# Performance work log

Measured on AMD Instinct MI355X. Metric: run time of the kernel, lower is better.

## Reference

```python
import jax, jax.numpy as jnp
import numpy as np

EPS = 1e-12  # F.normalize default eps (denominator = max(norm, eps))


def setup_inputs() -> dict:
    key = jax.random.key(0)
    ks = jax.random.split(key, 8)
    B, FIN, H, W = 4, 256, 64, 64
    N_MEM, SQ = 64, 16           # sqrt_fin = fin**0.5
    POS_CH = 2                    # PosEncoding concatenates one coord channel per dim
    CIN = FIN + POS_CH
    QK = N_MEM * SQ               # 1024
    # PosEncoding buffer: normalized coordinate grid in [-1, 1], shape [2, H, W]
    ys = jnp.linspace(-1.0, 1.0, H, dtype=jnp.float32)
    xs = jnp.linspace(-1.0, 1.0, W, dtype=jnp.float32)
    gy, gx = jnp.meshgrid(ys, xs, indexing='ij')
    pos = jnp.stack([gy, gx], axis=0)
    s = 0.02
    return {
        'x':    jax.random.normal(ks[0], (B, FIN, H, W), jnp.float32),
        'pos':  pos,
        'wq':   jax.random.normal(ks[1], (QK, CIN), jnp.float32) * s,
        'bq':   jnp.zeros((QK,), jnp.float32),
        'wk':   jax.random.normal(ks[2], (QK, CIN), jnp.float32) * s,
        'bk':   jnp.zeros((QK,), jnp.float32),
        'v':    jax.random.normal(ks[3], (N_MEM, FIN), jnp.float32) * s,
        'wout': jax.random.normal(ks[4], (FIN, FIN), jnp.float32) * s,
        'bout': jnp.zeros((FIN,), jnp.float32),
    }


def reference(x, pos, wq, bq, wk, bk, v, wout, bout):
    B, C, H, W = x.shape
    S = H * W
    n_mem, fin = v.shape
    sq = wq.shape[0] // n_mem
    # PosEncoding: concat coordinate channels
    posb = jnp.broadcast_to(pos[None], (B,) + pos.shape)
    xp = jnp.concatenate([x, posb], axis=1).reshape(B, C + pos.shape[0], S)
    # 1x1 conv projections (channel GEMMs)
    q = jnp.einsum('oc,bcs->bos', wq, xp) + bq[None, :, None]  # [B, n_mem*sq, S]
    k = jnp.einsum('oc,bcs->bos', wk, xp) + bk[None, :, None]
    q = q.reshape(B, n_mem, sq, S).transpose(0, 3, 1, 2)  # [B,S,m,sq]
    k = k.reshape(B, n_mem, sq, S).transpose(0, 3, 2, 1)  # [B,S,sq,m]
    # F.normalize: q over last dim (sqrt_fin), k over dim=1 (sqrt_fin)
    qn = q / jnp.maximum(jnp.linalg.norm(q, axis=-1, keepdims=True), EPS)
    kn = k / jnp.maximum(jnp.linalg.norm(k, axis=2, keepdims=True), EPS)
    # attn[b,s,m,n] = qn . kn ; dropout is identity in eval mode.
    # mean over memory slots m commutes with (attn @ v), so fuse:
    attn_mean = jnp.einsum('bsk,bskn->bsn', qn.mean(axis=2), kn)  # [B,S,n_mem]
    mem = attn_mean @ v                                            # [B,S,fin]
    mem = mem.transpose(0, 2, 1).reshape(B, fin, H, W)
    out = jnp.einsum('of,bfhw->bohw', wout, mem) + bout[None, :, None, None]
    return x + out
```

## Files before the change

kernel.cpp:

```cpp
#include <hip/hip_runtime.h>
#include <stdint.h>

#define EPSN 1e-12f

typedef float f32x16 __attribute__((ext_vector_type(16)));
typedef float f32x4 __attribute__((ext_vector_type(4)));
typedef __bf16 bf16x8 __attribute__((ext_vector_type(8)));

__device__ __forceinline__ unsigned short f2bf(float f) {
  union { float f; unsigned int u; } v; v.f = f;
  unsigned int u = v.u + 0x7FFFu + ((v.u >> 16) & 1u);
  return (unsigned short)(u >> 16);
}

#define NKS 17
#define WQF_OFF 0
#define WKF_OFF (32 * NKS * 64 * 8)
#define WVP_OFF (2 * 32 * NKS * 64 * 8)

__global__ __launch_bounds__(256) void prep_kernel(
    const float* __restrict__ wq, const float* __restrict__ bq,
    const float* __restrict__ wk, const float* __restrict__ bk,
    const float* __restrict__ v, const float* __restrict__ wout,
    unsigned short* __restrict__ wsp) {
  int bid = blockIdx.x;
  if (bid < 512) {
    int isK = bid >= 256;
    int ob = (bid & 255) * 4;
    const float* w = isK ? wk : wq;
    const float* bb = isK ? bk : bq;
    unsigned short* dst = wsp + (isK ? WKF_OFF : WQF_OFF);
    for (int i = threadIdx.x; i < 4 * 129; i += 256) {
      int r = i / 129, q = i - r * 129;
      int o = ob + r, k = q * 2;
      float2 w2 = *(const float2*)(w + o * 258 + k);
      int g = o >> 5, col = o & 31;
      int ks = k >> 4, hi = (k >> 3) & 1, j = k & 7;
      uint32_t pk = (uint32_t)f2bf(w2.x) | ((uint32_t)f2bf(w2.y) << 16);
      *(uint32_t*)(dst + (((g * NKS + ks) * 64 + hi * 32 + col) << 3) + j) = pk;
    }
    for (int i = threadIdx.x; i < 4 * 14; i += 256) {
      int r = i / 14, kk = 258 + (i - r * 14);
      int o = ob + r;
      int g = o >> 5, col = o & 31;
      int ks = kk >> 4, hi = (kk >> 3) & 1, j = kk & 7;
      dst[(((g * NKS + ks) * 64 + hi * 32 + col) << 3) + j] =
          (kk == 258) ? f2bf(bb[o]) : (unsigned short)0;
    }
  } else {
    int idx = (bid - 512) * 256 + threadIdx.x;
    int fc = idx & 15, m = (idx >> 4) & 63, o = idx >> 10;
    const f32x4* wo = (const f32x4*)(wout + o * 256 + fc * 16);
    const f32x4* vm = (const f32x4*)(v + m * 256 + fc * 16);
    float s = 0.f;
#pragma unroll
    for (int f = 0; f < 4; ++f) {
      f32x4 a = wo[f], bvv = vm[f];
      s += a[0]*bvv[0] + a[1]*bvv[1] + a[2]*bvv[2] + a[3]*bvv[3];
    }
    s += __shfl_xor(s, 1, 64);
    s += __shfl_xor(s, 2, 64);
    s += __shfl_xor(s, 4, 64);
    s += __shfl_xor(s, 8, 64);
    if (fc == 0) wsp[WVP_OFF + o * 64 + m] = f2bf(s);
  }
}

#define PXB 32
#define KP 296
#define QS 34
#define AT 76

__global__ __launch_bounds__(1024, 8) void fused_kernel(
    const float* __restrict__ x, const float* __restrict__ pos,
    const unsigned short* __restrict__ wsp, const float* __restrict__ bout,
    float* __restrict__ out) {
  __shared__ __align__(16) unsigned short xp[PXB * KP];
  __shared__ __align__(16) float qbarL[16 * QS];
  __shared__ __align__(16) unsigned short attnM[PXB * AT];
  __shared__ float boutL[256];

  const int tid = threadIdx.x;
  const int lane = tid & 63;
  const int wid = __builtin_amdgcn_readfirstlane(tid >> 6);
  const int px = lane & 31, q2 = lane >> 5;
  const int P0 = blockIdx.x * PXB;
  const int b = P0 >> 12, s0 = P0 & 4095;

  const int wtoff = (2 * wid) * NKS * 512 + lane * 8;
  const unsigned short* wqf = wsp + WQF_OFF + wtoff;
  const unsigned short* wkf = wsp + WKF_OFF + wtoff;

  uint32_t* xp32 = (uint32_t*)xp;
  {
    const float* xrow = x + b * 256 * 4096 + s0;
    float v0[4], v1[4];
#pragma unroll
    for (int it = 0; it < 4; ++it) {
      int item = tid + it * 1024;
      int pp = item & 31, dcol = item >> 5;
      v0[it] = xrow[(2 * dcol) * 4096 + pp];
      v1[it] = xrow[(2 * dcol + 1) * 4096 + pp];
    }
#pragma unroll
    for (int it = 0; it < 4; ++it) {
      int item = tid + it * 1024;
      int pp = item & 31, dcol = item >> 5;
      xp32[pp * 148 + dcol] =
          (uint32_t)f2bf(v0[it]) | ((uint32_t)f2bf(v1[it]) << 16);
    }
    if (tid < 256) {
      int pp = tid & 31, dcol = 128 + (tid >> 5);
      float t0 = 0.f, t1 = 0.f;
      if (dcol == 128) { t0 = pos[s0 + pp]; t1 = pos[4096 + s0 + pp]; }
      else if (dcol == 129) { t0 = 1.0f; }
      xp32[pp * 148 + dcol] = (uint32_t)f2bf(t0) | ((uint32_t)f2bf(t1) << 16);
    }
  }
  if (tid < 256) boutL[tid] = bout[tid];
  for (int i = tid; i < 16 * QS; i += 1024) qbarL[i] = 0.f;
  __syncthreads();

#define PHASE(WB) do {                                                    \
    _Pragma("unroll")                                                     \
    for (int ks = 0; ks < NKS; ++ks) {                                    \
      bf16x8 _A0 = *(const bf16x8*)((WB) + ks * 512);                     \
      bf16x8 _A1 = *(const bf16x8*)((WB) + NKS * 512 + ks * 512);         \
      bf16x8 _b0 = *(const bf16x8*)&xp[px * KP + ks * 16 + q2 * 8];       \
      acc0 = __builtin_amdgcn_mfma_f32_32x32x16_bf16(_A0, _b0, acc0, 0, 0, 0); \
      acc1 = __builtin_amdgcn_mfma_f32_32x32x16_bf16(_A1, _b0, acc1, 0, 0, 0); \
    }                                                                     \
  } while (0)

  f32x16 acc0 = (f32x16)0.f, acc1 = (f32x16)0.f;
  PHASE(wqf);

  {
    float qsum[8];
#pragma unroll
    for (int r = 0; r < 8; ++r) qsum[r] = 0.f;
#pragma unroll
    for (int ot = 0; ot < 2; ++ot) {
      const f32x16 a = ot ? acc1 : acc0;
      float s20 = 0.f, s21 = 0.f;
#pragma unroll
      for (int r = 0; r < 8; ++r) {
        s20 = fmaf(a[r], a[r], s20);
        s21 = fmaf(a[r + 8], a[r + 8], s21);
      }
      s20 += __shfl_xor(s20, 32, 64);
      s21 += __shfl_xor(s21, 32, 64);
      float i0 = 1.0f / fmaxf(sqrtf(s20), EPSN);
      float i1 = 1.0f / fmaxf(sqrtf(s21), EPSN);
#pragma unroll
      for (int r = 0; r < 8; ++r) qsum[r] += a[r] * i0 + a[r + 8] * i1;
    }
#pragma unroll
    for (int r = 0; r < 8; ++r) {
      int j = (r & 3) + ((r >> 2) << 3) + (q2 << 2);
      atomicAdd(&qbarL[j * QS + px], qsum[r] * (1.0f / 64.0f));
    }
  }

  acc0 = (f32x16)0.f; acc1 = (f32x16)0.f;
  PHASE(wkf);
  __syncthreads();

  {
    float qb[8];
#pragma unroll
    for (int r = 0; r < 8; ++r) {
      int j = (r & 3) + ((r >> 2) << 3) + (q2 << 2);
      qb[r] = qbarL[j * QS + px];
    }
#pragma unroll
    for (int ot = 0; ot < 2; ++ot) {
      const f32x16 a = ot ? acc1 : acc0;
      float s20 = 0.f, s21 = 0.f, sp0 = 0.f, sp1 = 0.f;
#pragma unroll
      for (int r = 0; r < 8; ++r) {
        s20 = fmaf(a[r], a[r], s20);         sp0 = fmaf(qb[r], a[r], sp0);
        s21 = fmaf(a[r + 8], a[r + 8], s21); sp1 = fmaf(qb[r], a[r + 8], sp1);
      }
      s20 += __shfl_xor(s20, 32, 64);
      s21 += __shfl_xor(s21, 32, 64);
      sp0 += __shfl_xor(sp0, 32, 64);
      sp1 += __shfl_xor(sp1, 32, 64);
      if (q2 == 0) {
        int m0 = wid * 4 + ot * 2;
        attnM[px * AT + m0]     = f2bf(sp0 / fmaxf(sqrtf(s20), EPSN));
        attnM[px * AT + m0 + 1] = f2bf(sp1 / fmaxf(sqrtf(s21), EPSN));
      }
    }
  }
  __syncthreads();

  if (wid < 8) {
    const int otile = wid;
    f32x16 e = (f32x16)0.f;
    const unsigned short* wv = wsp + WVP_OFF + (otile * 32 + px) * 64 + q2 * 8;
    const unsigned short* ab = &attnM[px * AT + q2 * 8];
#pragma unroll
    for (int ks = 0; ks < 4; ++ks) {
      bf16x8 av = *(const bf16x8*)(wv + ks * 16);
      bf16x8 bv = *(const bf16x8*)(ab + ks * 16);
      e = __builtin_amdgcn_mfma_f32_32x32x16_bf16(av, bv, e, 0, 0, 0);
    }
#pragma unroll
    for (int r = 0; r < 16; ++r) {
      const int o = otile * 32 + (r & 3) + ((r >> 2) << 3) + (q2 << 2);
      const int gi = (b * 256 + o) * 4096 + s0 + px;
      out[gi] = x[gi] + boutL[o] + e[r];
    }
  }
#undef PHASE
}

extern "C" void kernel_launch(void* const* d_in, const int* in_sizes, int n_in,
                              void* d_out, int out_size, void* d_ws, size_t ws_size,
                              hipStream_t stream) {
  const float* x    = (const float*)d_in[0];
  const float* pos  = (const float*)d_in[1];
  const float* wq   = (const float*)d_in[2];
  const float* bq   = (const float*)d_in[3];
  const float* wk   = (const float*)d_in[4];
  const float* bk   = (const float*)d_in[5];
  const float* v    = (const float*)d_in[6];
  const float* wout = (const float*)d_in[7];
  const float* bout = (const float*)d_in[8];
  float* out = (float*)d_out;
  unsigned short* wsp = (unsigned short*)d_ws;

  hipLaunchKernelGGL(prep_kernel, dim3(1536), dim3(256), 0, stream,
                     wq, bq, wk, bk, v, wout, wsp);
  hipLaunchKernelGGL(fused_kernel, dim3(512), dim3(1024), 0, stream,
                     x, pos, wsp, bout, out);
}
```

Before: 128.4 us.

## Merge weight-prep and fused kernels into one launch with a grid barrier

Folds the weight conversion and packing work into the main kernel. Each of the 512 blocks first does its share of the prep, then loads its x tile into shared memory, and all blocks then meet at a software grid barrier (an atomic counter on a global variable) before the MFMA phases. This removes one kernel launch and the gap between the two kernels, and overlaps the x loads with the prep. In exchange it depends on all 512 blocks being resident at once, or the spin barrier deadlocks, and it adds global atomic spinning.

```diff
diff --git a/kernel.cpp b/kernel.cpp
--- a/kernel.cpp
+++ b/kernel.cpp
@@ -18,19 +18,43 @@
 #define WKF_OFF (32 * NKS * 64 * 8)
 #define WVP_OFF (2 * 32 * NKS * 64 * 8)
 
-__global__ __launch_bounds__(256) void prep_kernel(
+__device__ uint32_t g_bar = 0;
+
+#define NBLK 512
+
+#define PXB 32
+#define KP 296
+#define QS 34
+#define AT 76
+
+__global__ __launch_bounds__(1024, 8) void mono_kernel(
+    const float* __restrict__ x, const float* __restrict__ pos,
     const float* __restrict__ wq, const float* __restrict__ bq,
     const float* __restrict__ wk, const float* __restrict__ bk,
     const float* __restrict__ v, const float* __restrict__ wout,
-    unsigned short* __restrict__ wsp) {
-  int bid = blockIdx.x;
-  if (bid < 512) {
+    const float* __restrict__ bout,
+    unsigned short* __restrict__ wsp, float* __restrict__ out) {
+  __shared__ __align__(16) unsigned short xp[PXB * KP];
+  __shared__ __align__(16) float qbarL[16 * QS];
+  __shared__ __align__(16) unsigned short attnM[PXB * AT];
+  __shared__ float boutL[256];
+
+  const int tid = threadIdx.x;
+  const int lane = tid & 63;
+  const int wid = __builtin_amdgcn_readfirstlane(tid >> 6);
+  const int px = lane & 31, q2 = lane >> 5;
+  const int bid = blockIdx.x;
+  const int P0 = bid * PXB;
+  const int b = P0 >> 12, s0 = P0 & 4095;
+
+  {
     int isK = bid >= 256;
     int ob = (bid & 255) * 4;
     const float* w = isK ? wk : wq;
     const float* bb = isK ? bk : bq;
     unsigned short* dst = wsp + (isK ? WKF_OFF : WQF_OFF);
-    for (int i = threadIdx.x; i < 4 * 129; i += 256) {
+    if (tid < 4 * 129) {
+      int i = tid;
       int r = i / 129, q = i - r * 129;
       int o = ob + r, k = q * 2;
       float2 w2 = *(const float2*)(w + o * 258 + k);
@@ -39,7 +63,8 @@
       uint32_t pk = (uint32_t)f2bf(w2.x) | ((uint32_t)f2bf(w2.y) << 16);
       *(uint32_t*)(dst + (((g * NKS + ks) * 64 + hi * 32 + col) << 3) + j) = pk;
     }
-    for (int i = threadIdx.x; i < 4 * 14; i += 256) {
+    if (tid >= 516 && tid < 516 + 4 * 14) {
+      int i = tid - 516;
       int r = i / 14, kk = 258 + (i - r * 14);
       int o = ob + r;
       int g = o >> 5, col = o & 31;
@@ -47,8 +72,9 @@
       dst[(((g * NKS + ks) * 64 + hi * 32 + col) << 3) + j] =
           (kk == 258) ? f2bf(bb[o]) : (unsigned short)0;
     }
-  } else {
-    int idx = (bid - 512) * 256 + threadIdx.x;
+  }
+  if (tid < 512) {
+    int idx = bid * 512 + tid;
     int fc = idx & 15, m = (idx >> 4) & 63, o = idx >> 10;
     const f32x4* wo = (const f32x4*)(wout + o * 256 + fc * 16);
     const f32x4* vm = (const f32x4*)(v + m * 256 + fc * 16);
@@ -64,32 +90,6 @@
     s += __shfl_xor(s, 8, 64);
     if (fc == 0) wsp[WVP_OFF + o * 64 + m] = f2bf(s);
   }
-}
-
-#define PXB 32
-#define KP 296
-#define QS 34
-#define AT 76
-
-__global__ __launch_bounds__(1024, 8) void fused_kernel(
-    const float* __restrict__ x, const float* __restrict__ pos,
-    const unsigned short* __restrict__ wsp, const float* __restrict__ bout,
-    float* __restrict__ out) {
-  __shared__ __align__(16) unsigned short xp[PXB * KP];
-  __shared__ __align__(16) float qbarL[16 * QS];
-  __shared__ __align__(16) unsigned short attnM[PXB * AT];
-  __shared__ float boutL[256];
-
-  const int tid = threadIdx.x;
-  const int lane = tid & 63;
-  const int wid = __builtin_amdgcn_readfirstlane(tid >> 6);
-  const int px = lane & 31, q2 = lane >> 5;
-  const int P0 = blockIdx.x * PXB;
-  const int b = P0 >> 12, s0 = P0 & 4095;
-
-  const int wtoff = (2 * wid) * NKS * 512 + lane * 8;
-  const unsigned short* wqf = wsp + WQF_OFF + wtoff;
-  const unsigned short* wkf = wsp + WKF_OFF + wtoff;
 
   uint32_t* xp32 = (uint32_t*)xp;
   {
@@ -119,7 +119,20 @@
   }
   if (tid < 256) boutL[tid] = bout[tid];
   for (int i = tid; i < 16 * QS; i += 1024) qbarL[i] = 0.f;
-  __syncthreads();
+
+  __syncthreads();
+  if (tid == 0) {
+    __threadfence();
+    uint32_t old = atomicAdd(&g_bar, 1u);
+    uint32_t target = ((old >> 9) + 1u) << 9;
+    while (atomicAdd(&g_bar, 0u) < target) __builtin_amdgcn_s_sleep(2);
+    __threadfence();
+  }
+  __syncthreads();
+
+  const int wtoff = (2 * wid) * NKS * 512 + lane * 8;
+  const unsigned short* wqf = wsp + WQF_OFF + wtoff;
+  const unsigned short* wkf = wsp + WKF_OFF + wtoff;
 
 #define PHASE(WB) do {                                                    \
     _Pragma("unroll")                                                     \
@@ -231,8 +244,6 @@
   float* out = (float*)d_out;
   unsigned short* wsp = (unsigned short*)d_ws;
 
-  hipLaunchKernelGGL(prep_kernel, dim3(1536), dim3(256), 0, stream,
-                     wq, bq, wk, bk, v, wout, wsp);
-  hipLaunchKernelGGL(fused_kernel, dim3(512), dim3(1024), 0, stream,
-                     x, pos, wsp, bout, out);
+  hipLaunchKernelGGL(mono_kernel, dim3(NBLK), dim3(1024), 0, stream,
+                     x, pos, wq, bq, wk, bk, v, wout, bout, wsp, out);
 }
```

New measurement: 174.5 us. +35.9%, slower.

## Fuse Q/K GEMM loops, vectorize x loads, reuse LDS x for residual

Applied to the files above, without the earlier changes.

The input tile is now loaded with vectorized nontemporal float4 loads. The Q and K projections run in one loop that prefetches the next weight fragments, and the K norms are computed before the barrier. The epilogue takes the residual x from the bf16 copy already in LDS instead of reading x from global memory again, and writes the output with nontemporal stores. This removes a second full read of x and improves MFMA issue. The trade-offs are a bf16-rounded residual, which may break tolerance, and a lower occupancy hint in launch bounds.

```diff
diff --git a/kernel.cpp b/kernel.cpp
--- a/kernel.cpp
+++ b/kernel.cpp
@@ -6,11 +6,16 @@
 typedef float f32x16 __attribute__((ext_vector_type(16)));
 typedef float f32x4 __attribute__((ext_vector_type(4)));
 typedef __bf16 bf16x8 __attribute__((ext_vector_type(8)));
+typedef unsigned short u16x4 __attribute__((ext_vector_type(4)));
 
 __device__ __forceinline__ unsigned short f2bf(float f) {
   union { float f; unsigned int u; } v; v.f = f;
   unsigned int u = v.u + 0x7FFFu + ((v.u >> 16) & 1u);
   return (unsigned short)(u >> 16);
+}
+__device__ __forceinline__ float bf2f(unsigned short h) {
+  union { float f; unsigned int u; } v; v.u = ((unsigned int)h) << 16;
+  return v.f;
 }
 
 #define NKS 17
@@ -71,7 +76,7 @@
 #define QS 34
 #define AT 76
 
-__global__ __launch_bounds__(1024, 8) void fused_kernel(
+__global__ __launch_bounds__(1024, 4) void fused_kernel(
     const float* __restrict__ x, const float* __restrict__ pos,
     const unsigned short* __restrict__ wsp, const float* __restrict__ bout,
     float* __restrict__ out) {
@@ -94,22 +99,18 @@
   uint32_t* xp32 = (uint32_t*)xp;
   {
     const float* xrow = x + b * 256 * 4096 + s0;
-    float v0[4], v1[4];
-#pragma unroll
-    for (int it = 0; it < 4; ++it) {
-      int item = tid + it * 1024;
-      int pp = item & 31, dcol = item >> 5;
-      v0[it] = xrow[(2 * dcol) * 4096 + pp];
-      v1[it] = xrow[(2 * dcol + 1) * 4096 + pp];
-    }
-#pragma unroll
-    for (int it = 0; it < 4; ++it) {
-      int item = tid + it * 1024;
-      int pp = item & 31, dcol = item >> 5;
+    int g = tid & 7, dcol = tid >> 3;
+    f32x4 lo = __builtin_nontemporal_load(
+        (const f32x4*)(xrow + (2 * dcol) * 4096 + 4 * g));
+    f32x4 hi = __builtin_nontemporal_load(
+        (const f32x4*)(xrow + (2 * dcol + 1) * 4096 + 4 * g));
+#pragma unroll
+    for (int j = 0; j < 4; ++j) {
+      int pp = 4 * g + j;
       xp32[pp * 148 + dcol] =
-          (uint32_t)f2bf(v0[it]) | ((uint32_t)f2bf(v1[it]) << 16);
-    }
-    if (tid < 256) {
+          (uint32_t)f2bf(lo[j]) | ((uint32_t)f2bf(hi[j]) << 16);
+    }
+    if (tid < 32 * 20) {
       int pp = tid & 31, dcol = 128 + (tid >> 5);
       float t0 = 0.f, t1 = 0.f;
       if (dcol == 128) { t0 = pos[s0 + pp]; t1 = pos[4096 + s0 + pp]; }
@@ -121,19 +122,35 @@
   for (int i = tid; i < 16 * QS; i += 1024) qbarL[i] = 0.f;
   __syncthreads();
 
-#define PHASE(WB) do {                                                    \
-    _Pragma("unroll")                                                     \
-    for (int ks = 0; ks < NKS; ++ks) {                                    \
-      bf16x8 _A0 = *(const bf16x8*)((WB) + ks * 512);                     \
-      bf16x8 _A1 = *(const bf16x8*)((WB) + NKS * 512 + ks * 512);         \
-      bf16x8 _b0 = *(const bf16x8*)&xp[px * KP + ks * 16 + q2 * 8];       \
-      acc0 = __builtin_amdgcn_mfma_f32_32x32x16_bf16(_A0, _b0, acc0, 0, 0, 0); \
-      acc1 = __builtin_amdgcn_mfma_f32_32x32x16_bf16(_A1, _b0, acc1, 0, 0, 0); \
-    }                                                                     \
-  } while (0)
-
-  f32x16 acc0 = (f32x16)0.f, acc1 = (f32x16)0.f;
-  PHASE(wqf);
+  f32x16 aq0 = (f32x16)0.f, aq1 = (f32x16)0.f,
+         ak0 = (f32x16)0.f, ak1 = (f32x16)0.f;
+  {
+    const unsigned short* bp = &xp[px * KP + q2 * 8];
+    bf16x8 q0c = *(const bf16x8*)(wqf);
+    bf16x8 q1c = *(const bf16x8*)(wqf + NKS * 512);
+    bf16x8 k0c = *(const bf16x8*)(wkf);
+    bf16x8 k1c = *(const bf16x8*)(wkf + NKS * 512);
+#pragma unroll 1
+    for (int i = 0; i < NKS - 1; ++i) {
+      bf16x8 q0n = *(const bf16x8*)(wqf + (i + 1) * 512);
+      bf16x8 q1n = *(const bf16x8*)(wqf + NKS * 512 + (i + 1) * 512);
+      bf16x8 k0n = *(const bf16x8*)(wkf + (i + 1) * 512);
+      bf16x8 k1n = *(const bf16x8*)(wkf + NKS * 512 + (i + 1) * 512);
+      bf16x8 b0 = *(const bf16x8*)(bp + i * 16);
+      aq0 = __builtin_amdgcn_mfma_f32_32x32x16_bf16(q0c, b0, aq0, 0, 0, 0);
+      aq1 = __builtin_amdgcn_mfma_f32_32x32x16_bf16(q1c, b0, aq1, 0, 0, 0);
+      ak0 = __builtin_amdgcn_mfma_f32_32x32x16_bf16(k0c, b0, ak0, 0, 0, 0);
+      ak1 = __builtin_amdgcn_mfma_f32_32x32x16_bf16(k1c, b0, ak1, 0, 0, 0);
+      q0c = q0n; q1c = q1n; k0c = k0n; k1c = k1n;
+    }
+    {
+      bf16x8 b0 = *(const bf16x8*)(bp + (NKS - 1) * 16);
+      aq0 = __builtin_amdgcn_mfma_f32_32x32x16_bf16(q0c, b0, aq0, 0, 0, 0);
+      aq1 = __builtin_amdgcn_mfma_f32_32x32x16_bf16(q1c, b0, aq1, 0, 0, 0);
+      ak0 = __builtin_amdgcn_mfma_f32_32x32x16_bf16(k0c, b0, ak0, 0, 0, 0);
+      ak1 = __builtin_amdgcn_mfma_f32_32x32x16_bf16(k1c, b0, ak1, 0, 0, 0);
+    }
+  }
 
   {
     float qsum[8];
@@ -141,7 +158,7 @@
     for (int r = 0; r < 8; ++r) qsum[r] = 0.f;
 #pragma unroll
     for (int ot = 0; ot < 2; ++ot) {
-      const f32x16 a = ot ? acc1 : acc0;
+      const f32x16 a = ot ? aq1 : aq0;
       float s20 = 0.f, s21 = 0.f;
 #pragma unroll
       for (int r = 0; r < 8; ++r) {
@@ -162,8 +179,21 @@
     }
   }
 
-  acc0 = (f32x16)0.f; acc1 = (f32x16)0.f;
-  PHASE(wkf);
+  float ki0[2], ki1[2];
+#pragma unroll
+  for (int ot = 0; ot < 2; ++ot) {
+    const f32x16 a = ot ? ak1 : ak0;
+    float s20 = 0.f, s21 = 0.f;
+#pragma unroll
+    for (int r = 0; r < 8; ++r) {
+      s20 = fmaf(a[r], a[r], s20);
+      s21 = fmaf(a[r + 8], a[r + 8], s21);
+    }
+    s20 += __shfl_xor(s20, 32, 64);
+    s21 += __shfl_xor(s21, 32, 64);
+    ki0[ot] = 1.0f / fmaxf(sqrtf(s20), EPSN);
+    ki1[ot] = 1.0f / fmaxf(sqrtf(s21), EPSN);
+  }
   __syncthreads();
 
   {
@@ -175,21 +205,19 @@
     }
 #pragma unroll
     for (int ot = 0; ot < 2; ++ot) {
-      const f32x16 a = ot ? acc1 : acc0;
-      float s20 = 0.f, s21 = 0.f, sp0 = 0.f, sp1 = 0.f;
+      const f32x16 a = ot ? ak1 : ak0;
+      float sp0 = 0.f, sp1 = 0.f;
 #pragma unroll
       for (int r = 0; r < 8; ++r) {
-        s20 = fmaf(a[r], a[r], s20);         sp0 = fmaf(qb[r], a[r], sp0);
-        s21 = fmaf(a[r + 8], a[r + 8], s21); sp1 = fmaf(qb[r], a[r + 8], sp1);
-      }
-      s20 += __shfl_xor(s20, 32, 64);
-      s21 += __shfl_xor(s21, 32, 64);
+        sp0 = fmaf(qb[r], a[r], sp0);
+        sp1 = fmaf(qb[r], a[r + 8], sp1);
+      }
       sp0 += __shfl_xor(sp0, 32, 64);
       sp1 += __shfl_xor(sp1, 32, 64);
       if (q2 == 0) {
         int m0 = wid * 4 + ot * 2;
-        attnM[px * AT + m0]     = f2bf(sp0 / fmaxf(sqrtf(s20), EPSN));
-        attnM[px * AT + m0 + 1] = f2bf(sp1 / fmaxf(sqrtf(s21), EPSN));
+        attnM[px * AT + m0]     = f2bf(sp0 * ki0[ot]);
+        attnM[px * AT + m0 + 1] = f2bf(sp1 * ki1[ot]);
       }
     }
   }
@@ -206,14 +234,19 @@
       bf16x8 bv = *(const bf16x8*)(ab + ks * 16);
       e = __builtin_amdgcn_mfma_f32_32x32x16_bf16(av, bv, e, 0, 0, 0);
     }
-#pragma unroll
-    for (int r = 0; r < 16; ++r) {
-      const int o = otile * 32 + (r & 3) + ((r >> 2) << 3) + (q2 << 2);
-      const int gi = (b * 256 + o) * 4096 + s0 + px;
-      out[gi] = x[gi] + boutL[o] + e[r];
-    }
-  }
-#undef PHASE
+    const unsigned short* xl = &xp[px * KP + otile * 32 + (q2 << 2)];
+#pragma unroll
+    for (int rq = 0; rq < 4; ++rq) {
+      u16x4 xq = *(const u16x4*)(xl + 8 * rq);
+#pragma unroll
+      for (int j = 0; j < 4; ++j) {
+        const int r = rq * 4 + j;
+        const int o = otile * 32 + j + (rq << 3) + (q2 << 2);
+        const int gi = (b * 256 + o) * 4096 + s0 + px;
+        __builtin_nontemporal_store(bf2f(xq[j]) + boutL[o] + e[r], &out[gi]);
+      }
+    }
+  }
 }
 
 extern "C" void kernel_launch(void* const* d_in, const int* in_sizes, int n_in,
```

Result: slower. 135.7 us (+5.7%).
